# Optimization experiments

Hardware: AMD Instinct MI355X
Metric: run time of the kernel (lower is better)

The kernel has to match this reference:

```python
import jax, jax.numpy as jnp
import numpy as np

B, N, P, S = 8, 4096, 16, 200
W_SPS, W_EXT, W_CUB, W_CD = 0.1, 0.1, 1.0, 1.0
EXIST_THRED = 24.0

# cube face constants (from Loss._init_buffers)
MASK_PROJECT = jnp.array([[0,1,1],[0,1,1],[1,0,1],[1,0,1],[1,1,0],[1,1,0]], jnp.float32)  # [6,3]
MASK_PLANE   = jnp.array([[1,0,0],[1,0,0],[0,1,0],[0,1,0],[0,0,1],[0,0,1]], jnp.float32)  # [6,3]
CUBE_NORMAL  = jnp.array([[-1,0,0],[1,0,0],[0,-1,0],[0,1,0],[0,0,-1],[0,0,1]], jnp.float32)  # [6,3]
CUBE_PLANES6 = jnp.tile(jnp.array([[-1.,-1.,-1.],[1.,1.,1.]], jnp.float32), (3,1))  # [6,3] rows -,+,-,+,-,+


def setup_inputs() -> dict:
    key = jax.random.key(0)
    ks = jax.random.split(key, 10)
    pc = jax.random.normal(ks[0], (B, N, 3), jnp.float32)
    normals = jax.random.normal(ks[1], (B, N, 3), jnp.float32)
    normals = normals / jnp.linalg.norm(normals, axis=-1, keepdims=True)
    trans = 0.1 * jax.random.normal(ks[2], (B, P, 3), jnp.float32)
    Q, _ = jnp.linalg.qr(jax.random.normal(ks[3], (B, P, 3, 3), jnp.float32))
    rotate = Q  # random orthonormal rotation-like matrices
    scale = jax.random.uniform(ks[4], (B, P, 3), jnp.float32, 0.1, 1.0)
    shape_eps = jax.random.uniform(ks[5], (B, P, 2), jnp.float32, 0.2, 1.8)
    exist = jax.random.uniform(ks[6], (B, P, 1), jnp.float32, 0.01, 0.99)
    aw = jax.random.uniform(ks[7], (B, N, P), jnp.float32)
    assign_matrix = aw / aw.sum(-1, keepdims=True)
    etas = jax.random.uniform(ks[8], (B, P, S), jnp.float32, -1.47, 1.47)
    omegas = jax.random.uniform(ks[9], (B, P, S), jnp.float32, -3.1, 3.1)
    return dict(pc=pc, normals=normals, trans=trans, rotate=rotate, scale=scale,
                shape_eps=shape_eps, exist=exist, assign_matrix=assign_matrix,
                etas=etas, omegas=omegas)


def transform_to_primitive_frame(x, trans, rotate):
    # x: [B,N,3], trans: [B,P,3], rotate: [B,P,3,3] -> R^T (x - t): [B,P,N,3]
    d = x[:, None, :, :] - trans[:, :, None, :]
    return jnp.einsum('bpji,bpnj->bpni', rotate, d)


def fexp(x, p):
    return jnp.sign(x) * jnp.abs(x) ** p


def sample_sq_points(scale, eps, etas, omegas):
    # scale [B,P,3], eps [B,P,2], etas/omegas [B,P,S] -> points [B,P,S,3]
    etas = jnp.where(etas == 0, etas + 1e-6, etas)
    omegas = jnp.where(omegas == 0, omegas + 1e-6, omegas)
    a1, a2, a3 = scale[..., 0:1], scale[..., 1:2], scale[..., 2:3]
    e1, e2 = eps[..., 0:1], eps[..., 1:2]
    ce, se = jnp.cos(etas), jnp.sin(etas)
    co, so = jnp.cos(omegas), jnp.sin(omegas)
    x = a1 * fexp(ce, e1) * fexp(co, e2)
    y = a2 * fexp(ce, e1) * fexp(so, e2)
    z = a3 * fexp(se, e1)
    clamp = lambda v: ((v > 0).astype(v.dtype) * 2 - 1) * jnp.maximum(jnp.abs(v), 1e-6)
    return jnp.stack([clamp(x), clamp(y), clamp(z)], -1)


def compute_cuboid_loss(pc_inver, normals_inver, scale, assign_matrix):
    pcN = jnp.transpose(pc_inver, (0, 2, 1, 3))       # [B,N,P,3]
    nN = jnp.transpose(normals_inver, (0, 2, 1, 3))   # [B,N,P,3]
    # cosine similarity against 6 unit face normals (eps=1e-4 clamp)
    nrm = jnp.maximum(jnp.linalg.norm(nN, axis=-1, keepdims=True), 1e-4)
    sim = jnp.einsum('bnpd,fd->bnpf', nN, CUBE_NORMAL) / nrm  # [B,N,P,6]
    idx = jnp.argmax(sim, axis=-1)                    # [B,N,P]
    s = scale[:, None, :, None, :]                    # [B,1,P,1,3]
    planes_scaled = CUBE_PLANES6[None, None, None] * s  # [B,1,P,6,3]
    pcp = pcN[:, :, :, None, :] * MASK_PROJECT + planes_scaled * MASK_PLANE  # [B,N,P,6,3]
    pcp = jnp.clip(pcp, -s, s)
    b, n, p = pcp.shape[:3]
    gidx = jnp.broadcast_to(idx[..., None, None], (b, n, p, 1, 3))
    proj = jnp.take_along_axis(pcp, gidx, axis=3)[:, :, :, 0, :]  # [B,N,P,3]
    diff = ((proj - pcN) ** 2).sum(-1)                # [B,N,P]
    return jnp.mean((diff * assign_matrix).sum(-1))


def compute_cd_loss(pc_inver, scale, shape_eps, etas, omegas, assign_matrix, exist):
    X = sample_sq_points(scale, shape_eps, etas, omegas)  # [B,P,S,3]
    # squared pairwise distances D[b,p,s,n] via ||x||^2+||y||^2-2xy
    D = ((X ** 2).sum(-1)[..., None]
         + (pc_inver ** 2).sum(-1)[:, :, None, :]
         - 2.0 * jnp.einsum('bpsd,bpnd->bpsn', X, pc_inver))
    D = jnp.maximum(D, 0.0)
    pcl_to_prim = D.min(axis=2)                       # [B,P,N]
    pcl_to_prim_loss = jnp.mean((jnp.transpose(pcl_to_prim, (0, 2, 1)) * assign_matrix).sum(-1))
    # original returns (pcl_to_prim_loss, pcl_to_prim_loss)
    return pcl_to_prim_loss, pcl_to_prim_loss


def compute_existence_loss(assign_matrix, exist):
    gt = jax.lax.stop_gradient((assign_matrix.sum(1) > EXIST_THRED).astype(jnp.float32))  # [B,P]
    p = exist[..., 0]
    bce = -(gt * jnp.maximum(jnp.log(p), -100.0) + (1.0 - gt) * jnp.maximum(jnp.log(1.0 - p), -100.0))
    return jnp.mean(bce)


def get_sparsity_loss(assign_matrix):
    num_points = assign_matrix.shape[1]
    norm_05 = jnp.sqrt(assign_matrix.sum(1) / num_points + 0.01).mean(1) ** 2  # [B]
    return jnp.mean(norm_05)


def reference(pc, normals, trans, rotate, scale, shape_eps, exist, assign_matrix, etas, omegas):
    etas = jax.lax.stop_gradient(etas)      # sampler output is detached in original
    omegas = jax.lax.stop_gradient(omegas)
    pc_inver = transform_to_primitive_frame(pc, trans, rotate)       # [B,P,N,3]
    normals_inver = transform_to_primitive_frame(normals, trans, rotate)
    cub = compute_cuboid_loss(pc_inver, normals_inver, scale, assign_matrix)
    p2p, prim2p = compute_cd_loss(pc_inver, scale, shape_eps, etas, omegas, assign_matrix, exist)
    cd = p2p + prim2p
    ext = compute_existence_loss(assign_matrix, exist)
    sps = get_sparsity_loss(assign_matrix)
    return W_CUB * cub + W_CD * cd + W_EXT * ext + W_SPS * sps
```

## Files before the change

kernel.cpp:

```cpp
#include <hip/hip_runtime.h>
#include <math.h>

#define BB 8
#define NN 4096
#define PP 16
#define SS 200
#define NCHUNK 4
#define NBLK (BB*PP*NCHUNK)


__global__ __launch_bounds__(256) void main_kernel(
    const float* __restrict__ pc, const float* __restrict__ normals,
    const float* __restrict__ trans, const float* __restrict__ rotate,
    const float* __restrict__ scale, const float* __restrict__ shape_eps,
    const float* __restrict__ assign,
    const float* __restrict__ etas, const float* __restrict__ omegas,
    float* __restrict__ cub_part, float* __restrict__ cd_part,
    float* __restrict__ colsum_part) {
    __shared__ float4 Xs[SS];
    __shared__ float rc[4], rd[4], ra[4];

    int blk = blockIdx.x;
    int chunk = blk & (NCHUNK-1);
    int bp = blk >> 2;
    int b = bp >> 4;
    int p = bp & 15;

    if (threadIdx.x < SS) {
        int idx = bp * SS + threadIdx.x;
        float eta = etas[idx];
        float om  = omegas[idx];
        if (eta == 0.f) eta = 1e-6f;
        if (om  == 0.f) om  = 1e-6f;
        float a1 = scale[bp*3+0], a2 = scale[bp*3+1], a3 = scale[bp*3+2];
        float e1 = shape_eps[bp*2+0], e2 = shape_eps[bp*2+1];
        float ce = cosf(eta), se = sinf(eta);
        float co = cosf(om),  so = sinf(om);
        auto fexp = [](float x, float pw) {
            float sg = (x > 0.f) ? 1.f : ((x < 0.f) ? -1.f : 0.f);
            return sg * powf(fabsf(x), pw);
        };
        float fce = fexp(ce, e1);
        float x = a1 * fce * fexp(co, e2);
        float y = a2 * fce * fexp(so, e2);
        float z = a3 * fexp(se, e1);
        auto clampv = [](float v) {
            return ((v > 0.f) ? 1.f : -1.f) * fmaxf(fabsf(v), 1e-6f);
        };
        x = clampv(x); y = clampv(y); z = clampv(z);
        float xsq = x*x + y*y + z*z;
        Xs[threadIdx.x] = make_float4(-2.f*x, -2.f*y, -2.f*z, xsq);
    }

    float tx = trans[bp*3+0], ty = trans[bp*3+1], tz = trans[bp*3+2];
    float R0 = rotate[bp*9+0], R1 = rotate[bp*9+1], R2 = rotate[bp*9+2];
    float R3 = rotate[bp*9+3], R4 = rotate[bp*9+4], R5 = rotate[bp*9+5];
    float R6 = rotate[bp*9+6], R7 = rotate[bp*9+7], R8 = rotate[bp*9+8];
    float sx = scale[bp*3+0], sy = scale[bp*3+1], sz = scale[bp*3+2];

    float y0[4], y1[4], y2[4], ysq[4], aw[4];
    float acc_cub = 0.f, acc_as = 0.f;
#pragma unroll
    for (int j = 0; j < 4; j++) {
        int n = chunk * 1024 + j * 256 + threadIdx.x;
        size_t base = ((size_t)b * NN + n) * 3;
        float px = pc[base+0], py = pc[base+1], pz = pc[base+2];
        float qx = normals[base+0], qy = normals[base+1], qz = normals[base+2];
        aw[j] = assign[((size_t)b * NN + n) * PP + p];

        float d0 = px - tx, d1 = py - ty, d2 = pz - tz;
        y0[j] = R0*d0 + R3*d1 + R6*d2;
        y1[j] = R1*d0 + R4*d1 + R7*d2;
        y2[j] = R2*d0 + R5*d1 + R8*d2;
        float e0 = qx - tx, e1 = qy - ty, e2 = qz - tz;
        float m0 = R0*e0 + R3*e1 + R6*e2;
        float m1 = R1*e0 + R4*e1 + R7*e2;
        float m2 = R2*e0 + R5*e1 + R8*e2;

        float rn = 1.f / fmaxf(sqrtf(m0*m0 + m1*m1 + m2*m2), 1e-4f);
        float s0 = -m0*rn, s1 = m0*rn, s2 = -m1*rn, s3 = m1*rn, s4 = -m2*rn, s5 = m2*rn;
        int fidx = 0; float best = s0;
        if (s1 > best) { best = s1; fidx = 1; }
        if (s2 > best) { best = s2; fidx = 2; }
        if (s3 > best) { best = s3; fidx = 3; }
        if (s4 > best) { best = s4; fidx = 4; }
        if (s5 > best) { best = s5; fidx = 5; }
        int axis = fidx >> 1;
        float sgn = (fidx & 1) ? 1.f : -1.f;
        float pjx = fminf(fmaxf(y0[j], -sx), sx);
        float pjy = fminf(fmaxf(y1[j], -sy), sy);
        float pjz = fminf(fmaxf(y2[j], -sz), sz);
        if (axis == 0)      pjx = sgn * sx;
        else if (axis == 1) pjy = sgn * sy;
        else                pjz = sgn * sz;
        float dxx = pjx - y0[j], dyy = pjy - y1[j], dzz = pjz - y2[j];
        acc_cub += (dxx*dxx + dyy*dyy + dzz*dzz) * aw[j];
        ysq[j] = y0[j]*y0[j] + y1[j]*y1[j] + y2[j]*y2[j];
        acc_as += aw[j];
    }

    __syncthreads();

    float mmA[4] = {1e30f, 1e30f, 1e30f, 1e30f};
    float mmB[4] = {1e30f, 1e30f, 1e30f, 1e30f};
#pragma unroll 4
    for (int s = 0; s < SS; s += 2) {
        float4 xa = Xs[s+0], xb = Xs[s+1];
#pragma unroll
        for (int j = 0; j < 4; j++) {
            mmA[j] = fminf(mmA[j], fmaf(xa.x, y0[j], fmaf(xa.y, y1[j], fmaf(xa.z, y2[j], xa.w))));
            mmB[j] = fminf(mmB[j], fmaf(xb.x, y0[j], fmaf(xb.y, y1[j], fmaf(xb.z, y2[j], xb.w))));
        }
    }
    float acc_cd = 0.f;
#pragma unroll
    for (int j = 0; j < 4; j++) {
        float mn = fminf(mmA[j], mmB[j]);
        acc_cd += fmaxf(mn + ysq[j], 0.f) * aw[j];
    }

#pragma unroll
    for (int off = 32; off > 0; off >>= 1) {
        acc_cub += __shfl_down(acc_cub, off, 64);
        acc_cd  += __shfl_down(acc_cd,  off, 64);
        acc_as  += __shfl_down(acc_as,  off, 64);
    }
    int wave = threadIdx.x >> 6, lane = threadIdx.x & 63;
    if (lane == 0) { rc[wave] = acc_cub; rd[wave] = acc_cd; ra[wave] = acc_as; }
    __syncthreads();
    if (threadIdx.x == 0) {
        cub_part[blk]    = rc[0]+rc[1]+rc[2]+rc[3];
        cd_part[blk]     = rd[0]+rd[1]+rd[2]+rd[3];
        colsum_part[blk] = ra[0]+ra[1]+ra[2]+ra[3];
    }
}

__global__ void finalize_kernel(const float* __restrict__ exist,
                                const float* __restrict__ cub_part,
                                const float* __restrict__ cd_part,
                                const float* __restrict__ colsum_part,
                                float* __restrict__ out) {
    int t = threadIdx.x;
    __shared__ float bce_s[128], sq_s[128], rcub[4], rcd[4];

    float c1 = cub_part[t] + cub_part[t + 256];
    float c2 = cd_part[t]  + cd_part[t + 256];
#pragma unroll
    for (int off = 32; off > 0; off >>= 1) {
        c1 += __shfl_down(c1, off, 64);
        c2 += __shfl_down(c2, off, 64);
    }
    int wave = t >> 6, lane = t & 63;
    if (lane == 0) { rcub[wave] = c1; rcd[wave] = c2; }

    if (t < 128) {
        float cs = colsum_part[t*4+0] + colsum_part[t*4+1]
                 + colsum_part[t*4+2] + colsum_part[t*4+3];
        float gt = (cs > 24.0f) ? 1.f : 0.f;
        float pe = exist[t];
        float lg  = fmaxf(logf(pe), -100.f);
        float lg1 = fmaxf(logf(1.f - pe), -100.f);
        bce_s[t] = -(gt * lg + (1.f - gt) * lg1);
        sq_s[t] = sqrtf(cs / (float)NN + 0.01f);
    }
    __syncthreads();
    if (t == 0) {
        float ext = 0.f;
        for (int i = 0; i < 128; i++) ext += bce_s[i];
        ext /= 128.f;
        float sps = 0.f;
        for (int bb = 0; bb < 8; bb++) {
            float mb = 0.f;
            for (int pp2 = 0; pp2 < 16; pp2++) mb += sq_s[bb*16 + pp2];
            mb /= 16.f;
            sps += mb * mb;
        }
        sps /= 8.f;
        float cub = (rcub[0]+rcub[1]+rcub[2]+rcub[3]) / (float)(BB * NN);
        float p2p = (rcd[0]+rcd[1]+rcd[2]+rcd[3]) / (float)(BB * NN);
        float cd  = 2.f * p2p;
        out[0] = 1.0f * cub + 1.0f * cd + 0.1f * ext + 0.1f * sps;
    }
}

extern "C" void kernel_launch(void* const* d_in, const int* in_sizes, int n_in,
                              void* d_out, int out_size, void* d_ws, size_t ws_size,
                              hipStream_t stream) {
    const float* pc        = (const float*)d_in[0];
    const float* normals   = (const float*)d_in[1];
    const float* trans     = (const float*)d_in[2];
    const float* rotate    = (const float*)d_in[3];
    const float* scale     = (const float*)d_in[4];
    const float* shape_eps = (const float*)d_in[5];
    const float* exist     = (const float*)d_in[6];
    const float* assign    = (const float*)d_in[7];
    const float* etas      = (const float*)d_in[8];
    const float* omegas    = (const float*)d_in[9];

    float* ws = (float*)d_ws;
    float* cub_part    = ws;
    float* cd_part     = ws + NBLK;
    float* colsum_part = ws + 2*NBLK;

    main_kernel<<<NBLK, 256, 0, stream>>>(
        pc, normals, trans, rotate, scale, shape_eps, assign, etas, omegas,
        cub_part, cd_part, colsum_part);
    finalize_kernel<<<1, 256, 0, stream>>>(
        exist, cub_part, cd_part, colsum_part, (float*)d_out);
}
```

Baseline: 89.18 us.

## Split primitive-sample min search across waves with LDS partial-min reduction

Raises the block count from 512 to 2048 so that each thread handles one point instead of four. Inside a block, the 200 sample points are split among the 4 waves, and each wave evaluates all 256 block points against its 50 samples. The per-wave minima are written to shared memory and combined with a final min reduction. This gives more parallelism and better latency hiding, at the cost of recomputing the sample points per block (four times as often), extra LDS traffic and syncs, and a larger finalize reduction.

```diff
diff --git a/kernel.cpp b/kernel.cpp
--- a/kernel.cpp
+++ b/kernel.cpp
@@ -5,8 +5,8 @@
 #define NN 4096
 #define PP 16
 #define SS 200
-#define NCHUNK 4
-#define NBLK (BB*PP*NCHUNK)
+#define SPLIT 50
+#define NBLK (BB*PP*16)
 
 
 __global__ __launch_bounds__(256) void main_kernel(
@@ -18,16 +18,19 @@
     float* __restrict__ cub_part, float* __restrict__ cd_part,
     float* __restrict__ colsum_part) {
     __shared__ float4 Xs[SS];
+    __shared__ float4 y_lds[256];
+    __shared__ float partial[4*256];
     __shared__ float rc[4], rd[4], ra[4];
 
     int blk = blockIdx.x;
-    int chunk = blk & (NCHUNK-1);
-    int bp = blk >> 2;
-    int b = bp >> 4;
-    int p = bp & 15;
-
-    if (threadIdx.x < SS) {
-        int idx = bp * SS + threadIdx.x;
+    int chunk = blk & 15;
+    int p = (blk >> 4) & 15;
+    int b = blk >> 8;
+    int bp = b * PP + p;
+    int t = threadIdx.x;
+
+    if (t < SS) {
+        int idx = bp * SS + t;
         float eta = etas[idx];
         float om  = omegas[idx];
         if (eta == 0.f) eta = 1e-6f;
@@ -48,8 +51,7 @@
             return ((v > 0.f) ? 1.f : -1.f) * fmaxf(fabsf(v), 1e-6f);
         };
         x = clampv(x); y = clampv(y); z = clampv(z);
-        float xsq = x*x + y*y + z*z;
-        Xs[threadIdx.x] = make_float4(-2.f*x, -2.f*y, -2.f*z, xsq);
+        Xs[t] = make_float4(-2.f*x, -2.f*y, -2.f*z, x*x + y*y + z*z);
     }
 
     float tx = trans[bp*3+0], ty = trans[bp*3+1], tz = trans[bp*3+2];
@@ -58,66 +60,71 @@
     float R6 = rotate[bp*9+6], R7 = rotate[bp*9+7], R8 = rotate[bp*9+8];
     float sx = scale[bp*3+0], sy = scale[bp*3+1], sz = scale[bp*3+2];
 
-    float y0[4], y1[4], y2[4], ysq[4], aw[4];
-    float acc_cub = 0.f, acc_as = 0.f;
-#pragma unroll
-    for (int j = 0; j < 4; j++) {
-        int n = chunk * 1024 + j * 256 + threadIdx.x;
-        size_t base = ((size_t)b * NN + n) * 3;
-        float px = pc[base+0], py = pc[base+1], pz = pc[base+2];
-        float qx = normals[base+0], qy = normals[base+1], qz = normals[base+2];
-        aw[j] = assign[((size_t)b * NN + n) * PP + p];
-
-        float d0 = px - tx, d1 = py - ty, d2 = pz - tz;
-        y0[j] = R0*d0 + R3*d1 + R6*d2;
-        y1[j] = R1*d0 + R4*d1 + R7*d2;
-        y2[j] = R2*d0 + R5*d1 + R8*d2;
-        float e0 = qx - tx, e1 = qy - ty, e2 = qz - tz;
-        float m0 = R0*e0 + R3*e1 + R6*e2;
-        float m1 = R1*e0 + R4*e1 + R7*e2;
-        float m2 = R2*e0 + R5*e1 + R8*e2;
-
-        float rn = 1.f / fmaxf(sqrtf(m0*m0 + m1*m1 + m2*m2), 1e-4f);
-        float s0 = -m0*rn, s1 = m0*rn, s2 = -m1*rn, s3 = m1*rn, s4 = -m2*rn, s5 = m2*rn;
-        int fidx = 0; float best = s0;
-        if (s1 > best) { best = s1; fidx = 1; }
-        if (s2 > best) { best = s2; fidx = 2; }
-        if (s3 > best) { best = s3; fidx = 3; }
-        if (s4 > best) { best = s4; fidx = 4; }
-        if (s5 > best) { best = s5; fidx = 5; }
-        int axis = fidx >> 1;
-        float sgn = (fidx & 1) ? 1.f : -1.f;
-        float pjx = fminf(fmaxf(y0[j], -sx), sx);
-        float pjy = fminf(fmaxf(y1[j], -sy), sy);
-        float pjz = fminf(fmaxf(y2[j], -sz), sz);
-        if (axis == 0)      pjx = sgn * sx;
-        else if (axis == 1) pjy = sgn * sy;
-        else                pjz = sgn * sz;
-        float dxx = pjx - y0[j], dyy = pjy - y1[j], dzz = pjz - y2[j];
-        acc_cub += (dxx*dxx + dyy*dyy + dzz*dzz) * aw[j];
-        ysq[j] = y0[j]*y0[j] + y1[j]*y1[j] + y2[j]*y2[j];
-        acc_as += aw[j];
-    }
-
-    __syncthreads();
-
-    float mmA[4] = {1e30f, 1e30f, 1e30f, 1e30f};
-    float mmB[4] = {1e30f, 1e30f, 1e30f, 1e30f};
-#pragma unroll 4
-    for (int s = 0; s < SS; s += 2) {
-        float4 xa = Xs[s+0], xb = Xs[s+1];
-#pragma unroll
-        for (int j = 0; j < 4; j++) {
-            mmA[j] = fminf(mmA[j], fmaf(xa.x, y0[j], fmaf(xa.y, y1[j], fmaf(xa.z, y2[j], xa.w))));
-            mmB[j] = fminf(mmB[j], fmaf(xb.x, y0[j], fmaf(xb.y, y1[j], fmaf(xb.z, y2[j], xb.w))));
-        }
-    }
-    float acc_cd = 0.f;
-#pragma unroll
-    for (int j = 0; j < 4; j++) {
-        float mn = fminf(mmA[j], mmB[j]);
-        acc_cd += fmaxf(mn + ysq[j], 0.f) * aw[j];
-    }
+    int n = chunk * 256 + t;
+    size_t base = ((size_t)b * NN + n) * 3;
+    float px = pc[base+0], py = pc[base+1], pz = pc[base+2];
+    float qx = normals[base+0], qy = normals[base+1], qz = normals[base+2];
+    float aw = assign[((size_t)b * NN + n) * PP + p];
+
+    float d0 = px - tx, d1 = py - ty, d2 = pz - tz;
+    float y0 = R0*d0 + R3*d1 + R6*d2;
+    float y1 = R1*d0 + R4*d1 + R7*d2;
+    float y2 = R2*d0 + R5*d1 + R8*d2;
+    float e0 = qx - tx, e1 = qy - ty, e2 = qz - tz;
+    float m0 = R0*e0 + R3*e1 + R6*e2;
+    float m1 = R1*e0 + R4*e1 + R7*e2;
+    float m2 = R2*e0 + R5*e1 + R8*e2;
+
+    float rn = 1.f / fmaxf(sqrtf(m0*m0 + m1*m1 + m2*m2), 1e-4f);
+    float s0 = -m0*rn, s1 = m0*rn, s2 = -m1*rn, s3 = m1*rn, s4 = -m2*rn, s5 = m2*rn;
+    int fidx = 0; float best = s0;
+    if (s1 > best) { best = s1; fidx = 1; }
+    if (s2 > best) { best = s2; fidx = 2; }
+    if (s3 > best) { best = s3; fidx = 3; }
+    if (s4 > best) { best = s4; fidx = 4; }
+    if (s5 > best) { best = s5; fidx = 5; }
+    int axis = fidx >> 1;
+    float sgn = (fidx & 1) ? 1.f : -1.f;
+    float pjx = fminf(fmaxf(y0, -sx), sx);
+    float pjy = fminf(fmaxf(y1, -sy), sy);
+    float pjz = fminf(fmaxf(y2, -sz), sz);
+    if (axis == 0)      pjx = sgn * sx;
+    else if (axis == 1) pjy = sgn * sy;
+    else                pjz = sgn * sz;
+    float dxx = pjx - y0, dyy = pjy - y1, dzz = pjz - y2;
+    float acc_cub = (dxx*dxx + dyy*dyy + dzz*dzz) * aw;
+    float ysq = y0*y0 + y1*y1 + y2*y2;
+
+    y_lds[t] = make_float4(y0, y1, y2, 0.f);
+    __syncthreads();
+
+    int w = t >> 6, l = t & 63;
+    float4 pA = y_lds[l], pB = y_lds[l+64], pC = y_lds[l+128], pD = y_lds[l+192];
+    float mmA[4] = {1e30f,1e30f,1e30f,1e30f};
+    float mmB[4] = {1e30f,1e30f,1e30f,1e30f};
+    int sbase = w * SPLIT;
+#pragma unroll 5
+    for (int s = sbase; s < sbase + SPLIT; s += 2) {
+        float4 xa = Xs[s], xb = Xs[s+1];
+        mmA[0] = fminf(mmA[0], fmaf(xa.x, pA.x, fmaf(xa.y, pA.y, fmaf(xa.z, pA.z, xa.w))));
+        mmA[1] = fminf(mmA[1], fmaf(xa.x, pB.x, fmaf(xa.y, pB.y, fmaf(xa.z, pB.z, xa.w))));
+        mmA[2] = fminf(mmA[2], fmaf(xa.x, pC.x, fmaf(xa.y, pC.y, fmaf(xa.z, pC.z, xa.w))));
+        mmA[3] = fminf(mmA[3], fmaf(xa.x, pD.x, fmaf(xa.y, pD.y, fmaf(xa.z, pD.z, xa.w))));
+        mmB[0] = fminf(mmB[0], fmaf(xb.x, pA.x, fmaf(xb.y, pA.y, fmaf(xb.z, pA.z, xb.w))));
+        mmB[1] = fminf(mmB[1], fmaf(xb.x, pB.x, fmaf(xb.y, pB.y, fmaf(xb.z, pB.z, xb.w))));
+        mmB[2] = fminf(mmB[2], fmaf(xb.x, pC.x, fmaf(xb.y, pC.y, fmaf(xb.z, pC.z, xb.w))));
+        mmB[3] = fminf(mmB[3], fmaf(xb.x, pD.x, fmaf(xb.y, pD.y, fmaf(xb.z, pD.z, xb.w))));
+    }
+    partial[w*256 + l      ] = fminf(mmA[0], mmB[0]);
+    partial[w*256 + l + 64 ] = fminf(mmA[1], mmB[1]);
+    partial[w*256 + l + 128] = fminf(mmA[2], mmB[2]);
+    partial[w*256 + l + 192] = fminf(mmA[3], mmB[3]);
+    __syncthreads();
+
+    float mn = fminf(fminf(partial[t], partial[256 + t]),
+                     fminf(partial[512 + t], partial[768 + t]));
+    float acc_cd = fmaxf(mn + ysq, 0.f) * aw;
+    float acc_as = aw;
 
 #pragma unroll
     for (int off = 32; off > 0; off >>= 1) {
@@ -125,10 +132,9 @@
         acc_cd  += __shfl_down(acc_cd,  off, 64);
         acc_as  += __shfl_down(acc_as,  off, 64);
     }
-    int wave = threadIdx.x >> 6, lane = threadIdx.x & 63;
-    if (lane == 0) { rc[wave] = acc_cub; rd[wave] = acc_cd; ra[wave] = acc_as; }
-    __syncthreads();
-    if (threadIdx.x == 0) {
+    if (l == 0) { rc[w] = acc_cub; rd[w] = acc_cd; ra[w] = acc_as; }
+    __syncthreads();
+    if (t == 0) {
         cub_part[blk]    = rc[0]+rc[1]+rc[2]+rc[3];
         cd_part[blk]     = rd[0]+rd[1]+rd[2]+rd[3];
         colsum_part[blk] = ra[0]+ra[1]+ra[2]+ra[3];
@@ -143,8 +149,12 @@
     int t = threadIdx.x;
     __shared__ float bce_s[128], sq_s[128], rcub[4], rcd[4];
 
-    float c1 = cub_part[t] + cub_part[t + 256];
-    float c2 = cd_part[t]  + cd_part[t + 256];
+    float c1 = 0.f, c2 = 0.f;
+#pragma unroll
+    for (int i = 0; i < 8; i++) {
+        c1 += cub_part[t + 256*i];
+        c2 += cd_part[t + 256*i];
+    }
 #pragma unroll
     for (int off = 32; off > 0; off >>= 1) {
         c1 += __shfl_down(c1, off, 64);
@@ -154,8 +164,9 @@
     if (lane == 0) { rcub[wave] = c1; rcd[wave] = c2; }
 
     if (t < 128) {
-        float cs = colsum_part[t*4+0] + colsum_part[t*4+1]
-                 + colsum_part[t*4+2] + colsum_part[t*4+3];
+        float cs = 0.f;
+#pragma unroll
+        for (int c = 0; c < 16; c++) cs += colsum_part[t*16 + c];
         float gt = (cs > 24.0f) ? 1.f : 0.f;
         float pe = exist[t];
         float lg  = fmaxf(logf(pe), -100.f);
```

After: 95.61 us. 1.07x slower.
